# Kernel tuning notes

Measured on AMD Instinct MI355X. Metric: run time of the kernel, lower is better.

## Reference

```python
import jax, jax.numpy as jnp
import numpy as np

D_MODEL = 1024
NUM_HEADS = 16
D_K = D_MODEL // NUM_HEADS          # 64
D_ROPE = int(D_K * 0.5)             # 32
ROPE_BASE = 10000.0


def _rope(x):
    # x: [L, B, H, D_K]; rotate first D_ROPE features, pass the rest through.
    L = x.shape[0]
    d = D_ROPE
    theta = 1.0 / (ROPE_BASE ** (jnp.arange(0, d, 2, dtype=jnp.float32) / d))  # [d/2]
    idx_theta = jnp.arange(L, dtype=jnp.float32)[:, None] * theta[None, :]     # [L, d/2]
    idx_theta2 = jnp.concatenate([idx_theta, idx_theta], axis=-1)              # [L, d]
    cos = jnp.cos(idx_theta2)[:, None, None, :].astype(x.dtype)
    sin = jnp.sin(idx_theta2)[:, None, None, :].astype(x.dtype)
    x_rope, x_pass = x[..., :d], x[..., d:]
    neg_half = jnp.concatenate([-x_rope[..., d // 2:], x_rope[..., :d // 2]], axis=-1)
    x_rope = x_rope * cos + neg_half * sin
    return jnp.concatenate([x_rope, x_pass], axis=-1)


def setup_inputs() -> dict:
    key = jax.random.key(0)
    k1, k2 = jax.random.split(key)
    L, B = 2048, 2
    x = jax.random.normal(k1, (L, B, D_MODEL), dtype=jnp.float32)
    # xavier_uniform-like init for in_proj_weight [3*d_model, d_model]
    limit = float(np.sqrt(6.0 / (3 * D_MODEL + D_MODEL)))
    in_proj_weight = jax.random.uniform(k2, (3 * D_MODEL, D_MODEL),
                                        minval=-limit, maxval=limit, dtype=jnp.float32)
    return {"x": x, "in_proj_weight": in_proj_weight}


def reference(x, in_proj_weight):
    L, B, _ = x.shape
    # fused QKV projection: [L, B, 3*d_model]
    qkv = jnp.einsum('ed,lbd->lbe', in_proj_weight, x)
    # NOTE: faithful to original quirk — reshape to per-head blocks of 3*d_k,
    # then chunk along last dim.
    qkv = qkv.reshape(L, B, NUM_HEADS, 3 * D_K)
    q, k, v = qkv[..., :D_K], qkv[..., D_K:2 * D_K], qkv[..., 2 * D_K:]
    q = _rope(q)
    k = _rope(k)
    # [L,B,H,dk] -> [H,B,L,dk]
    q, k, v = (jnp.swapaxes(t, 0, 2) for t in (q, k, v))
    scale = 1.0 / jnp.sqrt(jnp.asarray(D_K, dtype=x.dtype))
    scores = jnp.einsum('hbqd,hbkd->hbqk', q, k) * scale      # [H,B,L,L]
    attn = jax.nn.softmax(scores, axis=-1)
    out = jnp.einsum('hbqk,hbkd->hbqd', attn, v)              # [H,B,L,dk]
    out = jnp.transpose(out, (1, 2, 0, 3)).reshape(B, L, D_MODEL)
    return jnp.swapaxes(out, 0, 1)                            # [L,B,D] (batch_first falsy)
```

## Files before the change

### kernel.cpp

```cpp
#include <hip/hip_runtime.h>
#include <hip/hip_bf16.h>
#include <cstdint>
#include <cstddef>

#define L_SEQ 2048
#define BATCH 2
#define DM 1024
#define NH 16
#define DK 64
#define QKV_N 3072
#define QK_N 2048
#define NX (4096 * 1024)
#define NW (3072 * 1024)

typedef short short8_t __attribute__((ext_vector_type(8)));
typedef short short4_t __attribute__((ext_vector_type(4)));
typedef float f32x4 __attribute__((ext_vector_type(4)));

#define MFMA32(a, b, c) __builtin_amdgcn_mfma_f32_16x16x32_bf16(a, b, c, 0, 0, 0)
#define MFMA16(a, b, c) __builtin_amdgcn_mfma_f32_16x16x16bf16_1k(a, b, c, 0, 0, 0)
#define EXP2(x) __builtin_amdgcn_exp2f(x)

static __device__ __forceinline__ unsigned pk2(float a, float b) {
  __hip_bfloat162 h = __float22bfloat162_rn(make_float2(a, b));
  union { __hip_bfloat162 h; unsigned u; } v;
  v.h = h;
  return v.u;
}

static __device__ __forceinline__ void async_copy16(const unsigned short* g,
                                                    unsigned short* l) {
  __builtin_amdgcn_global_load_lds(
      (const __attribute__((address_space(1))) unsigned int*)g,
      (__attribute__((address_space(3))) unsigned int*)l, 16, 0, 0);
}

__global__ __launch_bounds__(256) void cast_kernel(
    const float* __restrict__ X, const float* __restrict__ W,
    unsigned short* __restrict__ dst) {
  const int e = (blockIdx.x * 256 + threadIdx.x) * 8;
  const float* src = (e < NX) ? &X[e] : &W[e - NX];
  const float4 v0 = *(const float4*)src;
  const float4 v1 = *(const float4*)(src + 4);
  union { short8_t s8; unsigned u[4]; } o;
  o.u[0] = pk2(v0.x, v0.y);
  o.u[1] = pk2(v0.z, v0.w);
  o.u[2] = pk2(v1.x, v1.y);
  o.u[3] = pk2(v1.z, v1.w);
  *(short8_t*)&dst[e] = o.s8;
}

__global__ __launch_bounds__(256) void qkv_gemm_bf16(
    const unsigned short* __restrict__ Xb, const unsigned short* __restrict__ Wb,
    unsigned short* __restrict__ qkb, unsigned short* __restrict__ vtb) {
  __shared__ __align__(16) unsigned short As[2][128 * 32];
  __shared__ __align__(16) unsigned short Bs[2][128 * 32];
  const int t = threadIdx.x;
  const int w = t >> 6;
  const int lane = t & 63;
  const int L16 = lane & 15;
  const int quad = lane >> 4;
  const int hid = blockIdx.y * 24 + blockIdx.x;
  const int id = (hid & 7) * 96 + (hid >> 3);
  const int n0 = (id % 24) * 128;
  const int m0 = (id / 24) * 128;
  const int wm = w & 1;
  const int wn = w >> 1;

  const int c0 = w * 128 + lane;
  const int c1 = c0 + 64;
  const unsigned short* gA0 = Xb + (size_t)(m0 + (c0 >> 2)) * 1024 + (c0 & 3) * 8;
  const unsigned short* gA1 = Xb + (size_t)(m0 + (c1 >> 2)) * 1024 + (c1 & 3) * 8;
  const unsigned short* gB0 = Wb + (size_t)(n0 + (c0 >> 2)) * 1024 + (c0 & 3) * 8;
  const unsigned short* gB1 = Wb + (size_t)(n0 + (c1 >> 2)) * 1024 + (c1 & 3) * 8;

  f32x4 acc[4][4];
#pragma unroll
  for (int i = 0; i < 4; ++i)
#pragma unroll
    for (int j = 0; j < 4; ++j) acc[i][j] = (f32x4){0.f, 0.f, 0.f, 0.f};

  async_copy16(gA0, &As[0][w * 1024]);
  async_copy16(gA1, &As[0][w * 1024 + 512]);
  async_copy16(gB0, &Bs[0][w * 1024]);
  async_copy16(gB1, &Bs[0][w * 1024 + 512]);

#define GBODY(K0, BUF)                                                        \
  {                                                                           \
    __syncthreads();           \
    if ((K0) + 32 < 1024) {                                                   \
      async_copy16(gA0 + (K0) + 32, &As[(BUF) ^ 1][w * 1024]);                \
      async_copy16(gA1 + (K0) + 32, &As[(BUF) ^ 1][w * 1024 + 512]);          \
      async_copy16(gB0 + (K0) + 32, &Bs[(BUF) ^ 1][w * 1024]);                \
      async_copy16(gB1 + (K0) + 32, &Bs[(BUF) ^ 1][w * 1024 + 512]);          \
    }                                                                         \
    short8_t af[4], bfr[4];                                                   \
    _Pragma("unroll") for (int mt = 0; mt < 4; ++mt)                          \
        af[mt] = *(const short8_t*)                                           \
            &As[BUF][(wm * 64 + mt * 16 + L16) * 32 + quad * 8];              \
    _Pragma("unroll") for (int nt = 0; nt < 4; ++nt)                          \
        bfr[nt] = *(const short8_t*)                                          \
            &Bs[BUF][(wn * 64 + nt * 16 + L16) * 32 + quad * 8];              \
    _Pragma("unroll") for (int mt = 0; mt < 4; ++mt)                          \
        _Pragma("unroll") for (int nt = 0; nt < 4; ++nt)                      \
            acc[mt][nt] = MFMA32(af[mt], bfr[nt], acc[mt][nt]);               \
  }

  for (int k0 = 0; k0 < 1024; k0 += 64) {
    GBODY(k0, 0)
    GBODY(k0 + 32, 1)
  }

  const int chunk = (n0 >> 6) + wn;
  const int h = chunk / 3;
  const int type = chunk % 3;
  if (type == 2) {
#pragma unroll
    for (int mt = 0; mt < 4; ++mt) {
      const int mbase = m0 + wm * 64 + mt * 16 + quad * 4;
      const int lb = mbase >> 1;
#pragma unroll
      for (int nt = 0; nt < 4; ++nt) {
        const int d = L16 + nt * 16;
        const size_t r0 = ((size_t)(h * 64 + d)) * 2048 + lb;
        const size_t r1 = ((size_t)((16 + h) * 64 + d)) * 2048 + lb;
        *(unsigned*)&vtb[r0] = pk2(acc[mt][nt][0], acc[mt][nt][2]);
        *(unsigned*)&vtb[r1] = pk2(acc[mt][nt][1], acc[mt][nt][3]);
      }
    }
  } else {
    const float qs = (type == 0) ? 0.18033688011112042f : 1.0f;
    const int cbase = h * 128 + type * 64 + L16 * 2;
    const float theta = exp2f(-(float)L16 * 0.8304820237218405f);
#pragma unroll
    for (int mt = 0; mt < 4; ++mt) {
      const int mbase = m0 + wm * 64 + mt * 16 + quad * 4;
      const int lb = mbase >> 1;
      float sv[2], cv[2];
      __sincosf((float)lb * theta, &sv[0], &cv[0]);
      __sincosf((float)(lb + 1) * theta, &sv[1], &cv[1]);
#pragma unroll
      for (int reg = 0; reg < 4; ++reg) {
        const int li = reg >> 1;
        const float v0 = acc[mt][0][reg], v1 = acc[mt][1][reg];
        const float r0 = v0 * cv[li] - v1 * sv[li];
        const float r1 = v1 * cv[li] + v0 * sv[li];
        const size_t r = (size_t)(mbase + reg) * QK_N + cbase;
        *(unsigned*)&qkb[r]      = pk2(r0 * qs, r1 * qs);
        *(unsigned*)&qkb[r + 32] = pk2(acc[mt][2][reg] * qs,
                                       acc[mt][3][reg] * qs);
      }
    }
  }
}

__global__ __launch_bounds__(256, 2) void attn_mfma_kernel(
    const unsigned short* __restrict__ qkb,
    const unsigned short* __restrict__ vtb, float* __restrict__ out) {
  __shared__ __align__(16) unsigned short Ks[3][4096];
  __shared__ __align__(16) unsigned short Vs[3][4096];

  const int t = threadIdx.x;
  const int w = t >> 6;
  const int lane = t & 63;
  const int L16 = lane & 15;
  const int quad = lane >> 4;
  const int hid = blockIdx.y * 16 + blockIdx.x;
  const int bh = (hid & 7) * 4 + ((hid >> 3) & 3);
  const int l0 = (hid >> 5) * 128;
  const int b = bh & 1;
  const int h = bh >> 1;
  const int vh = b * 16 + h;

  const f32x4 z4 = {0.f, 0.f, 0.f, 0.f};

  short8_t bq[2][2];
#pragma unroll
  for (int mt = 0; mt < 2; ++mt)
#pragma unroll
    for (int kc = 0; kc < 2; ++kc)
      bq[mt][kc] = *(const short8_t*)
          &qkb[((size_t)((l0 + w * 32 + mt * 16 + L16) * 2 + b)) * QK_N +
               h * 128 + kc * 32 + quad * 8];

  f32x4 oc[2][4];
  float l_part[2] = {0.f, 0.f};
#pragma unroll
  for (int mt = 0; mt < 2; ++mt)
#pragma unroll
    for (int dt = 0; dt < 4; ++dt) oc[mt][dt] = z4;

  const int kr0 = w * 8 + (lane >> 3);
  const int kcs = ((lane & 7) ^ (lane >> 3)) * 8;
  const unsigned short* gK0 =
      qkb + (size_t)(kr0 * 2 + b) * QK_N + h * 128 + 64 + kcs;
  const unsigned short* gK1 = gK0 + (size_t)64 * QK_N;
  const size_t kstep = (size_t)128 * QK_N;

  const unsigned short* gV0 =
      vtb + ((size_t)(vh * 64 + w * 8 + (lane >> 3))) * 2048 +
      (((lane & 7) ^ (lane >> 3)) << 3);
  const unsigned short* gV1 = gV0 + (size_t)32 * 2048;

#define STAGE(KT, B)                                                          \
  {                                                                           \
    async_copy16(gK0 + (size_t)(KT) * kstep, &Ks[B][w * 512]);                \
    async_copy16(gK1 + (size_t)(KT) * kstep, &Ks[B][w * 512 + 2048]);         \
    async_copy16(gV0 + (KT) * 64, &Vs[B][w * 512]);                           \
    async_copy16(gV1 + (KT) * 64, &Vs[B][w * 512 + 2048]);                    \
  }

  STAGE(0, 0)
  STAGE(1, 1)

  const int rsw = (L16 & 7);
  const int vswz = (L16 & 7) << 3;

  int cur = 0;
  for (int kt = 0; kt < 32; ++kt) {
    asm volatile("s_waitcnt vmcnt(4)\n\ts_barrier" ::: "memory");
    if (kt + 2 < 32) {
      const int nb = (cur + 2 >= 3) ? cur - 1 : cur + 2;
      STAGE(kt + 2, nb)
    }
    __builtin_amdgcn_s_setprio(1);
#pragma unroll
    for (int nt = 0; nt < 4; ++nt) {
      const short8_t ak0 = *(const short8_t*)
          &Ks[cur][(nt * 16 + L16) * 64 + (quad ^ rsw) * 8];
      const short8_t ak1 = *(const short8_t*)
          &Ks[cur][(nt * 16 + L16) * 64 + ((quad + 4) ^ rsw) * 8];
      f32x4 t0 = MFMA32(ak0, bq[0][0], z4);
      const f32x4 s0v = MFMA32(ak1, bq[0][1], t0);
      f32x4 t1 = MFMA32(ak0, bq[1][0], z4);
      const f32x4 s1v = MFMA32(ak1, bq[1][1], t1);
      float p0 = EXP2(s0v[0]), p1 = EXP2(s0v[1]);
      float p2 = EXP2(s0v[2]), p3 = EXP2(s0v[3]);
      l_part[0] += (p0 + p1) + (p2 + p3);
      union { short4_t s4; unsigned u[2]; } pu0;
      pu0.u[0] = pk2(p0, p1);
      pu0.u[1] = pk2(p2, p3);
      float q0 = EXP2(s1v[0]), q1 = EXP2(s1v[1]);
      float q2 = EXP2(s1v[2]), q3 = EXP2(s1v[3]);
      l_part[1] += (q0 + q1) + (q2 + q3);
      union { short4_t s4; unsigned u[2]; } pu1;
      pu1.u[0] = pk2(q0, q1);
      pu1.u[1] = pk2(q2, q3);
#pragma unroll
      for (int dt = 0; dt < 4; ++dt) {
        const short4_t vf = *(const short4_t*)
            &Vs[cur][(dt * 16 + L16) * 64 + ((nt * 16 + quad * 4) ^ vswz)];
        oc[0][dt] = MFMA16(vf, pu0.s4, oc[0][dt]);
        oc[1][dt] = MFMA16(vf, pu1.s4, oc[1][dt]);
      }
    }
    __builtin_amdgcn_s_setprio(0);
    cur = (cur == 2) ? 0 : cur + 1;
  }

#pragma unroll
  for (int mt = 0; mt < 2; ++mt) {
    float l = l_part[mt];
    l += __shfl_xor(l, 16);
    l += __shfl_xor(l, 32);
    const float inv = 1.f / l;
    const int qrow = l0 + w * 32 + mt * 16 + L16;
    const size_t rbase = ((size_t)(qrow * 2 + b)) * DM + h * DK;
#pragma unroll
    for (int dt = 0; dt < 4; ++dt) {
      *(float4*)&out[rbase + dt * 16 + quad * 4] =
          make_float4(oc[mt][dt][0] * inv, oc[mt][dt][1] * inv,
                      oc[mt][dt][2] * inv, oc[mt][dt][3] * inv);
    }
  }
}

extern "C" void kernel_launch(void* const* d_in, const int* in_sizes, int n_in,
                              void* d_out, int out_size, void* d_ws,
                              size_t ws_size, hipStream_t stream) {
  const float* x = (const float*)d_in[0];
  const float* w = (const float*)d_in[1];
  float* out = (float*)d_out;
  unsigned short* bf = (unsigned short*)d_ws;
  unsigned short* Xb = bf;
  unsigned short* Wb = bf + NX;
  unsigned short* qkb =
      (unsigned short*)((char*)d_ws + (16u << 20));
  unsigned short* vtb =
      (unsigned short*)((char*)d_ws + (32u << 20));

  cast_kernel<<<(NX + NW) / (256 * 8), 256, 0, stream>>>(x, w, bf);
  qkv_gemm_bf16<<<dim3(QKV_N / 128, (L_SEQ * BATCH) / 128), 256, 0, stream>>>(
      Xb, Wb, qkb, vtb);
  attn_mfma_kernel<<<dim3(L_SEQ / 128, NH * BATCH), 256, 0, stream>>>(qkb, vtb,
                                                                      out);
}
```

Before: 156.3 us.

## Triple-buffer QKV GEMM loads with partial vmcnt waits and fix final attention wait

The QKV GEMM moves from double buffering guarded by __syncthreads to a three-stage LDS ring. Each step waits with vmcnt(4), so the next tile's async global-to-LDS copies stay in flight while the current tile is computed. This aims to hide global load latency in the projection GEMM. It raises LDS use per block from 32KB to 48KB, which may lower occupancy. The attention loop now waits for vmcnt(0) on its last iteration and adds lgkmcnt(0) to the barrier, so the final stage is fully landed before use.

After: 171.2 us. +9.6%, slower.

```diff
diff --git a/kernel.cpp b/kernel.cpp
--- a/kernel.cpp
+++ b/kernel.cpp
@@ -20,6 +20,11 @@
 #define MFMA32(a, b, c) __builtin_amdgcn_mfma_f32_16x16x32_bf16(a, b, c, 0, 0, 0)
 #define MFMA16(a, b, c) __builtin_amdgcn_mfma_f32_16x16x16bf16_1k(a, b, c, 0, 0, 0)
 #define EXP2(x) __builtin_amdgcn_exp2f(x)
+
+#define WAITK4_BAR() \
+  asm volatile("s_waitcnt vmcnt(4) lgkmcnt(0)\n\ts_barrier" ::: "memory")
+#define WAITK0_BAR() \
+  asm volatile("s_waitcnt vmcnt(0) lgkmcnt(0)\n\ts_barrier" ::: "memory")
 
 static __device__ __forceinline__ unsigned pk2(float a, float b) {
   __hip_bfloat162 h = __float22bfloat162_rn(make_float2(a, b));
@@ -53,8 +58,8 @@
 __global__ __launch_bounds__(256) void qkv_gemm_bf16(
     const unsigned short* __restrict__ Xb, const unsigned short* __restrict__ Wb,
     unsigned short* __restrict__ qkb, unsigned short* __restrict__ vtb) {
-  __shared__ __align__(16) unsigned short As[2][128 * 32];
-  __shared__ __align__(16) unsigned short Bs[2][128 * 32];
+  __shared__ __align__(16) unsigned short As[3][128 * 32];
+  __shared__ __align__(16) unsigned short Bs[3][128 * 32];
   const int t = threadIdx.x;
   const int w = t >> 6;
   const int lane = t & 63;
@@ -80,36 +85,46 @@
 #pragma unroll
     for (int j = 0; j < 4; ++j) acc[i][j] = (f32x4){0.f, 0.f, 0.f, 0.f};
 
-  async_copy16(gA0, &As[0][w * 1024]);
-  async_copy16(gA1, &As[0][w * 1024 + 512]);
-  async_copy16(gB0, &Bs[0][w * 1024]);
-  async_copy16(gB1, &Bs[0][w * 1024 + 512]);
-
-#define GBODY(K0, BUF)                                                        \
+#define GSTAGE(KS, B)                                                         \
   {                                                                           \
-    __syncthreads();           \
-    if ((K0) + 32 < 1024) {                                                   \
-      async_copy16(gA0 + (K0) + 32, &As[(BUF) ^ 1][w * 1024]);                \
-      async_copy16(gA1 + (K0) + 32, &As[(BUF) ^ 1][w * 1024 + 512]);          \
-      async_copy16(gB0 + (K0) + 32, &Bs[(BUF) ^ 1][w * 1024]);                \
-      async_copy16(gB1 + (K0) + 32, &Bs[(BUF) ^ 1][w * 1024 + 512]);          \
-    }                                                                         \
+    async_copy16(gA0 + (KS) * 32, &As[B][w * 1024]);                          \
+    async_copy16(gA1 + (KS) * 32, &As[B][w * 1024 + 512]);                    \
+    async_copy16(gB0 + (KS) * 32, &Bs[B][w * 1024]);                          \
+    async_copy16(gB1 + (KS) * 32, &Bs[B][w * 1024 + 512]);                    \
+  }
+
+#define GCOMP(B)                                                              \
+  {                                                                           \
     short8_t af[4], bfr[4];                                                   \
     _Pragma("unroll") for (int mt = 0; mt < 4; ++mt)                          \
         af[mt] = *(const short8_t*)                                           \
-            &As[BUF][(wm * 64 + mt * 16 + L16) * 32 + quad * 8];              \
+            &As[B][(wm * 64 + mt * 16 + L16) * 32 + quad * 8];                \
     _Pragma("unroll") for (int nt = 0; nt < 4; ++nt)                          \
         bfr[nt] = *(const short8_t*)                                          \
-            &Bs[BUF][(wn * 64 + nt * 16 + L16) * 32 + quad * 8];              \
+            &Bs[B][(wn * 64 + nt * 16 + L16) * 32 + quad * 8];                \
     _Pragma("unroll") for (int mt = 0; mt < 4; ++mt)                          \
         _Pragma("unroll") for (int nt = 0; nt < 4; ++nt)                      \
             acc[mt][nt] = MFMA32(af[mt], bfr[nt], acc[mt][nt]);               \
   }
 
-  for (int k0 = 0; k0 < 1024; k0 += 64) {
-    GBODY(k0, 0)
-    GBODY(k0 + 32, 1)
-  }
+  GSTAGE(0, 0)
+  GSTAGE(1, 1)
+
+  for (int ks = 0; ks < 30; ks += 3) {
+    WAITK4_BAR();
+    GSTAGE(ks + 2, 2)
+    GCOMP(0)
+    WAITK4_BAR();
+    GSTAGE(ks + 3, 0)
+    GCOMP(1)
+    WAITK4_BAR();
+    GSTAGE(ks + 4, 1)
+    GCOMP(2)
+  }
+  WAITK4_BAR();
+  GCOMP(0)
+  WAITK0_BAR();
+  GCOMP(1)
 
   const int chunk = (n0 >> 6) + wn;
   const int h = chunk / 3;
@@ -218,7 +233,11 @@
 
   int cur = 0;
   for (int kt = 0; kt < 32; ++kt) {
-    asm volatile("s_waitcnt vmcnt(4)\n\ts_barrier" ::: "memory");
+    if (kt < 31) {
+      WAITK4_BAR();
+    } else {
+      WAITK0_BAR();
+    }
     if (kt + 2 < 32) {
       const int nb = (cur + 2 >= 3) ? cur - 1 : cur + 2;
       STAGE(kt + 2, nb)
```
